# Performance work log

Hardware: AMD Instinct MI355X
Metric: run time of the kernel (lower is better)

Reference implementation:

```python
import jax, jax.numpy as jnp
import numpy as np

DIM = 384
HEADS = 12
HEAD_DIM = DIM // HEADS
WS = 7          # window_size
SS = 3          # shift_size (SW-MSA)
DIM_FF = 4 * DIM
EPS = 1e-5


def _rel_pos_index():
    coords = np.stack(np.meshgrid(np.arange(WS), np.arange(WS), indexing='ij'))
    cf = coords.reshape(2, -1)                       # (2, 49)
    rel = cf[:, :, None] - cf[:, None, :]            # (2, 49, 49)
    rel = rel.transpose(1, 2, 0).astype(np.int64)
    rel[:, :, 0] += WS - 1
    rel[:, :, 1] += WS - 1
    rel[:, :, 0] *= 2 * WS - 1
    return rel.sum(-1)                               # (49, 49)


def _attn_mask(Hp, Wp):
    # cyclic-shift mask, computed on static shapes with numpy
    img = np.zeros((Hp, Wp))
    slices = (slice(0, -WS), slice(-WS, -SS), slice(-SS, None))
    cnt = 0
    for hs in slices:
        for ws_ in slices:
            img[hs, ws_] = cnt
            cnt += 1
    mw = img.reshape(Hp // WS, WS, Wp // WS, WS).transpose(0, 2, 1, 3).reshape(-1, WS * WS)
    am = mw[:, None, :] - mw[:, :, None]             # unsqueeze(1) - unsqueeze(2)
    am = np.where(am != 0, -100.0, 0.0)
    return jnp.asarray(am, jnp.float32)              # (nW, 49, 49)


def _ln(x, g, b):
    mu = jnp.mean(x, -1, keepdims=True)
    var = jnp.mean(jnp.square(x - mu), -1, keepdims=True)
    return (x - mu) * jax.lax.rsqrt(var + EPS) * g + b


def setup_inputs() -> dict:
    key = jax.random.key(0)
    ks = jax.random.split(key, 8)
    B, H, W = 32, 56, 56
    s = 0.02
    return {
        'x': jax.random.normal(ks[0], (B, H * W, DIM), jnp.float32),
        'H': H, 'W': W,
        'rel_idx': jnp.asarray(_rel_pos_index(), jnp.int32),
        'rpb_table': jax.random.normal(ks[1], ((2 * WS - 1) ** 2, HEADS), jnp.float32) * s,
        'qkv_w': jax.random.normal(ks[2], (DIM, 3 * DIM), jnp.float32) * s,
        'proj_w': jax.random.normal(ks[3], (DIM, DIM), jnp.float32) * s,
        'proj_b': jnp.zeros((DIM,), jnp.float32),
        'norm1_g': jnp.ones((DIM,), jnp.float32),
        'norm1_b': jnp.zeros((DIM,), jnp.float32),
        'norm2_g': jnp.ones((DIM,), jnp.float32),
        'norm2_b': jnp.zeros((DIM,), jnp.float32),
        'ffn_w1': jax.random.normal(ks[4], (DIM, DIM_FF), jnp.float32) * s,
        'ffn_b1': jnp.zeros((DIM_FF,), jnp.float32),
        'ffn_w2': jax.random.normal(ks[5], (DIM_FF, DIM), jnp.float32) * s,
        'ffn_b2': jnp.zeros((DIM,), jnp.float32),
    }


def reference(x, H, W, rel_idx, rpb_table, qkv_w, proj_w, proj_b,
              norm1_g, norm1_b, norm2_g, norm2_b,
              ffn_w1, ffn_b1, ffn_w2, ffn_b2):
    B, L, C = x.shape
    shortcut = x
    h = _ln(x, norm1_g, norm1_b).reshape(B, H, W, C)

    pad_b = (WS - H % WS) % WS
    pad_r = (WS - W % WS) % WS
    if pad_b > 0 or pad_r > 0:
        h = jnp.pad(h, ((0, 0), (0, pad_b), (0, pad_r), (0, 0)))
    Hp, Wp = H + pad_b, W + pad_r

    if SS > 0:
        h = jnp.roll(h, (-SS, -SS), axis=(1, 2))

    # window partition -> (B*nW, 49, C)
    nHw, nWw = Hp // WS, Wp // WS
    win = h.reshape(B, nHw, WS, nWw, WS, C).transpose(0, 1, 3, 2, 4, 5)
    win = win.reshape(-1, WS * WS, C)
    Bw, N = win.shape[0], WS * WS

    # window attention
    qkv = (win @ qkv_w).reshape(Bw, N, 3, HEADS, HEAD_DIM)
    q, k, v = [qkv[:, :, i].transpose(0, 2, 1, 3) for i in range(3)]  # (Bw, heads, N, hd)
    attn = jnp.einsum('bhnd,bhmd->bhnm', q, k) / np.sqrt(HEAD_DIM)

    bias = rpb_table[rel_idx]                      # (N, N, heads)
    attn = attn + bias.transpose(2, 0, 1)[None]

    if SS > 0:
        mask = _attn_mask(Hp, Wp)                  # (nW, N, N)
        nW = mask.shape[0]
        attn = attn.reshape(B, nW, HEADS, N, N) + mask[None, :, None]
        attn = attn.reshape(Bw, HEADS, N, N)

    attn = jax.nn.softmax(attn, axis=-1)
    out = jnp.einsum('bhnm,bhmd->bnhd', attn, v).reshape(Bw, N, C)
    out = out @ proj_w + proj_b

    # window reverse
    out = out.reshape(B, nHw, nWw, WS, WS, C).transpose(0, 1, 3, 2, 4, 5)
    out = out.reshape(B, Hp, Wp, C)
    if SS > 0:
        out = jnp.roll(out, (SS, SS), axis=(1, 2))
    if pad_b > 0 or pad_r > 0:
        out = out[:, :H, :W, :]

    h = shortcut + out.reshape(B, H * W, C)
    ff = _ln(h, norm2_g, norm2_b)
    ff = jax.nn.gelu(ff @ ffn_w1 + ffn_b1, approximate=False) @ ffn_w2 + ffn_b2
    return h + ff
```

## Files before the change

### kernel.cpp

```cpp
#include <hip/hip_runtime.h>

#define DEV __device__ __forceinline__

typedef __bf16 bf16x8 __attribute__((ext_vector_type(8)));
typedef float  f32x4  __attribute__((ext_vector_type(4)));
typedef unsigned short u16x8 __attribute__((ext_vector_type(8)));
typedef unsigned short u16x4 __attribute__((ext_vector_type(4)));
typedef long  longx2 __attribute__((ext_vector_type(2)));

DEV float b2f(unsigned short u) {
    unsigned int t = ((unsigned int)u) << 16;
    return __uint_as_float(t);
}
DEV unsigned short f2b(float f) {
    unsigned int u = __float_as_uint(f);
    unsigned int r = (u + 0x7FFFu + ((u >> 16) & 1u)) >> 16;
    return (unsigned short)r;
}
DEV unsigned char f2f8(float f) {
    return (unsigned char)(__builtin_amdgcn_cvt_pk_fp8_f32(f, f, 0, false) & 0xff);
}

DEV int kpos(int c) {
    int s = (c >> 3) & 7;
    return (c & ~63) | ((((s & 3) << 1) | (s >> 2)) << 3) | (c & 7);
}

DEV void gload_lds16(const void* g, void* l) {
    __builtin_amdgcn_global_load_lds(
        (const __attribute__((address_space(1))) void*)g,
        (__attribute__((address_space(3))) void*)l, 16, 0, 0);
}

DEV size_t win_to_tok(int row) {
    int w = row / 49, t = row - w * 49;
    int b  = w >> 6, widx = w & 63;
    int wi = widx >> 3, wj = widx & 7;
    int ti = t / 7, tj = t - ti * 7;
    int hh = wi * 7 + ti + 3; if (hh >= 56) hh -= 56;
    int ww = wj * 7 + tj + 3; if (ww >= 56) ww -= 56;
    return (size_t)b * 3136 + (size_t)hh * 56 + ww;
}

__global__ void tokmap_build(int* __restrict__ tm, int T) {
    int i = blockIdx.x * 256 + threadIdx.x;
    if (i < T) tm[i] = (int)win_to_tok(i);
}

__global__ void wprep8(const float* __restrict__ src, unsigned char* __restrict__ dst,
                       int K, int N) {
    int idx = blockIdx.x * 256 + threadIdx.x;
    if (idx >= K * N) return;
    int k = idx / N, n = idx - k * N;
    dst[(size_t)n * K + kpos(k)] = f2f8(src[idx]);
}

__global__ void btab_build(const int* __restrict__ rel_idx, const float* __restrict__ rpb,
                           float* __restrict__ tab) {
    int idx = blockIdx.x * 256 + threadIdx.x;
    if (idx >= 4 * 12 * 64 * 64) return;
    int col = idx & 63, row = (idx >> 6) & 63;
    int h = (idx >> 12) % 12, cls = idx / (12 * 4096);
    float v;
    if (row >= 49 || col >= 49) {
        v = -10000.f;
    } else {
        v = rpb[rel_idx[row * 49 + col] * 12 + h];
        int ti = row / 7, tj = row - (row / 7) * 7;
        int si = col / 7, sj = col - (col / 7) * 7;
        int lq = ((cls & 2) ? (ti < 4 ? 1 : 2) : 0) * 3 + ((cls & 1) ? (tj < 4 ? 1 : 2) : 0);
        int lk = ((cls & 2) ? (si < 4 ? 1 : 2) : 0) * 3 + ((cls & 1) ? (sj < 4 ? 1 : 2) : 0);
        if (lq != lk) v -= 100.f;
    }
    tab[idx] = v;
}

template <int REMAP>
__global__ __launch_bounds__(256) void ln_kernel(const float* __restrict__ x,
                                                 const float* __restrict__ g,
                                                 const float* __restrict__ b,
                                                 unsigned char* __restrict__ out,
                                                 int rows) {
    int r = blockIdx.x * 4 + (threadIdx.x >> 6);
    int lane = threadIdx.x & 63;
    if (r >= rows) return;
    size_t src = REMAP ? win_to_tok(r) : (size_t)r;
    const float* xp = x + src * 384;
    float v[6];
    float s = 0.f;
#pragma unroll
    for (int i = 0; i < 6; ++i) { v[i] = xp[i * 64 + lane]; s += v[i]; }
#pragma unroll
    for (int off = 32; off; off >>= 1) s += __shfl_xor(s, off, 64);
    float mu = s * (1.f / 384.f);
    float q = 0.f;
#pragma unroll
    for (int i = 0; i < 6; ++i) { float d = v[i] - mu; q += d * d; }
#pragma unroll
    for (int off = 32; off; off >>= 1) q += __shfl_xor(q, off, 64);
    float inv = rsqrtf(q * (1.f / 384.f) + 1e-5f);
    unsigned char* op = out + (size_t)r * 384;
#pragma unroll
    for (int i = 0; i < 6; ++i) {
        int c = i * 64 + lane;
        op[kpos(c)] = f2f8((v[i] - mu) * inv * g[c] + b[c]);
    }
}

template <int MODE>
__global__ __launch_bounds__(512, 2) void gemm_f8_fullk(const unsigned char* __restrict__ A,
                                                        const unsigned char* __restrict__ Bt,
                                                        int M, int N, int K,
                                                        const float* __restrict__ bias,
                                                        const float* __restrict__ resid,
                                                        const int* __restrict__ tokmap,
                                                        unsigned char* __restrict__ outb8,
                                                        float* __restrict__ outf) {
    __shared__ unsigned char Als[64 * 384];
    __shared__ unsigned char Bls[128 * 384];
    const int tid = threadIdx.x;
    const int wid = tid >> 6, lane = tid & 63;
    const int ntile = N >> 7;

    int bid = blockIdx.x;
    int nwg = gridDim.x;
    int swb = ((nwg & 7) == 0) ? ((bid & 7) * (nwg >> 3) + (bid >> 3)) : bid;
    const int mt = swb / ntile, nt = swb - mt * ntile;

    const unsigned char* Abase = A  + (size_t)(mt * 64) * K;
    const unsigned char* Bbase = Bt + (size_t)(nt * 128) * K;

    {
        int rB = tid >> 2;
        int gpB = (tid & 3) ^ ((rB >> 1) & 3);
#pragma unroll
        for (int kb = 0; kb < 6; ++kb)
            gload_lds16(Bbase + (size_t)rB * K + kb * 64 + gpB * 16, &Bls[kb * 8192 + tid * 16]);
        if (tid < 256) {
            int rA = tid >> 2;
            int gpA = (tid & 3) ^ ((rA >> 1) & 3);
#pragma unroll
            for (int kb = 0; kb < 6; ++kb)
                gload_lds16(Abase + (size_t)rA * K + kb * 64 + gpA * 16, &Als[kb * 4096 + tid * 16]);
        }
    }
    asm volatile("s_waitcnt vmcnt(0)" ::: "memory");
    __builtin_amdgcn_s_barrier();

    const int fr = lane & 15, kq = lane >> 4;
    const int cb = (kq ^ ((fr >> 1) & 3)) << 4;

    f32x4 acc[4] = {};
#pragma unroll
    for (int kb = 0; kb < 6; ++kb) {
        longx2 a[4], b;
        b = *(const longx2*)(&Bls[kb * 8192 + (wid * 16 + fr) * 64 + cb]);
#pragma unroll
        for (int m = 0; m < 4; ++m)
            a[m] = *(const longx2*)(&Als[kb * 4096 + (m * 16 + fr) * 64 + cb]);
#pragma unroll
        for (int ks = 0; ks < 2; ++ks)
#pragma unroll
            for (int m = 0; m < 4; ++m)
                acc[m] = __builtin_amdgcn_mfma_f32_16x16x32_fp8_fp8(b[ks], a[m][ks], acc[m], 0, 0, 0);
    }

    const int row0 = mt * 64;
    const int col0 = nt * 128 + wid * 16;
    const int rl = lane & 15;
    const int cq = (lane >> 4) << 2;
    const int col = col0 + cq;
#pragma unroll
    for (int m = 0; m < 4; ++m) {
        int row = row0 + m * 16 + rl;
        f32x4 v = acc[m];
        if constexpr (MODE == 0) {
            int pk = 0;
            pk = __builtin_amdgcn_cvt_pk_fp8_f32(v[0], v[1], pk, false);
            pk = __builtin_amdgcn_cvt_pk_fp8_f32(v[2], v[3], pk, true);
            *(int*)(outb8 + (size_t)row * N + col) = pk;
        } else if constexpr (MODE == 1) {
            size_t o = (size_t)tokmap[row] * 384 + col;
            f32x4 rv = *(const f32x4*)&resid[o];
            f32x4 bb = *(const f32x4*)&bias[col];
            f32x4 ov = rv + v + bb;
            *(f32x4*)&outf[o] = ov;
        } else {
            f32x4 bb = *(const f32x4*)&bias[col];
            float g4[4];
#pragma unroll
            for (int r = 0; r < 4; ++r) {
                float t2 = v[r] + bb[r];
                float e  = __expf(-1.702f * t2);
                g4[r] = t2 * __builtin_amdgcn_rcpf(1.f + e);
            }
            int pk = 0;
            pk = __builtin_amdgcn_cvt_pk_fp8_f32(g4[0], g4[1], pk, false);
            pk = __builtin_amdgcn_cvt_pk_fp8_f32(g4[2], g4[3], pk, true);
            *(int*)(outb8 + (size_t)row * N + kpos(col)) = pk;
        }
    }
}

template <int NBUF, int DEPTH, int MINW>
__global__ __launch_bounds__(256, MINW) void gemm_f8_ring(const unsigned char* __restrict__ A,
                                                          const unsigned char* __restrict__ Bt,
                                                          int M, int N, int K,
                                                          const float* __restrict__ bias,
                                                          const float* __restrict__ resid,
                                                          float* __restrict__ outf) {
    static_assert(NBUF >= DEPTH + 2, "ring too small");
    __shared__ unsigned char As[NBUF][128 * 64];
    __shared__ unsigned char Bs[NBUF][128 * 64];
    const int tid = threadIdx.x;
    const int wid = tid >> 6, lane = tid & 63;
    const int ntile = N >> 7;

    int bid = blockIdx.x;
    int nwg = gridDim.x;
    int swb = ((nwg & 7) == 0) ? ((bid & 7) * (nwg >> 3) + (bid >> 3)) : bid;
    const int mt = swb / ntile, nt = swb - mt * ntile;
    const int wr = wid >> 1, wc = wid & 1;

    f32x4 acc[4][4] = {};

    const unsigned char* Abase = A  + (size_t)(mt * 128) * K;
    const unsigned char* Bbase = Bt + (size_t)(nt * 128) * K;

    auto stage = [&](int buf, int k0) {
#pragma unroll
        for (int j = 0; j < 2; ++j) {
            int r  = j * 64 + (tid >> 2);
            int gp = (tid & 3) ^ ((r >> 1) & 3);
            gload_lds16(Abase + (size_t)r * K + k0 + gp * 16, &As[buf][j * 4096 + tid * 16]);
            gload_lds16(Bbase + (size_t)r * K + k0 + gp * 16, &Bs[buf][j * 4096 + tid * 16]);
        }
    };

    const int fr = lane & 15, kq = lane >> 4;
    const int rowA = wr * 64 + fr;
    const int rowB = wc * 64 + fr;
    const int cb = (kq ^ ((fr >> 1) & 3)) << 4;

    const int nk = K >> 6;
    stage(0, 0);
    if (nk > 1) stage(1, 64);

    for (int t = 0; t < nk; ++t) {
        const int cur = t % NBUF;
        if (t + DEPTH < nk) {
            stage((t + DEPTH) % NBUF, (t + DEPTH) << 6);
            asm volatile("s_waitcnt vmcnt(8)" ::: "memory");
        } else if (t + 1 < nk) {
            asm volatile("s_waitcnt vmcnt(4)" ::: "memory");
        } else {
            asm volatile("s_waitcnt vmcnt(0)" ::: "memory");
        }
        __builtin_amdgcn_s_barrier();

        longx2 a[4], b[4];
#pragma unroll
        for (int m = 0; m < 4; ++m)
            a[m] = *(const longx2*)(&As[cur][(rowA + m * 16) * 64 + cb]);
#pragma unroll
        for (int n = 0; n < 4; ++n)
            b[n] = *(const longx2*)(&Bs[cur][(rowB + n * 16) * 64 + cb]);
#pragma unroll
        for (int ks = 0; ks < 2; ++ks)
#pragma unroll
            for (int m = 0; m < 4; ++m)
#pragma unroll
                for (int n = 0; n < 4; ++n)
                    acc[m][n] = __builtin_amdgcn_mfma_f32_16x16x32_fp8_fp8(b[n][ks], a[m][ks], acc[m][n], 0, 0, 0);

        asm volatile("s_waitcnt lgkmcnt(0)" ::: "memory");
    }

    const int row0 = mt * 128 + wr * 64;
    const int col0 = nt * 128 + wc * 64;
    const int rl = lane & 15;
    const int cq = (lane >> 4) << 2;
#pragma unroll
    for (int m = 0; m < 4; ++m) {
        int row = row0 + m * 16 + rl;
#pragma unroll
        for (int n = 0; n < 4; ++n) {
            int col = col0 + n * 16 + cq;
            f32x4 v = acc[m][n];
            size_t o = (size_t)row * N + col;
            f32x4 rv = *(const f32x4*)&resid[o];
            f32x4 bb = *(const f32x4*)&bias[col];
            f32x4 ov = rv + v + bb;
            *(f32x4*)&outf[o] = ov;
        }
    }
}

__global__ __launch_bounds__(256, 2) void attn_kernel(const unsigned char* __restrict__ QKV8,
                                                      const float* __restrict__ Btab,
                                                      unsigned char* __restrict__ O8) {
    __shared__ char lds[8192 + 16384 + 32768];
    char* Kl = lds;
    char* Vl = lds + 8192;
    char* Pl = lds + 24576;

    const int w   = blockIdx.x;
    const int tid = threadIdx.x, wid = tid >> 6, lane = tid & 63;
    const int fr  = lane & 15, kq = lane >> 4;
    const size_t base = (size_t)w * 49 * 1152;
    const int widx = w & 63, wi = widx >> 3, wj = widx & 7;
    const int cls = ((wi == 7) ? 2 : 0) | ((wj == 7) ? 1 : 0);
    const float* tb = Btab + (size_t)cls * 12 * 4096;
    constexpr float SCL = 0.17677669529663687f;

    for (int R = 0; R < 3; ++R) {
        if (R) __syncthreads();
        {
            f32x4 z = {};
#pragma unroll
            for (int j = 0; j < 6; ++j) *(f32x4*)(lds + j * 4096 + tid * 16) = z;
        }
        __syncthreads();
        {
            int hh = tid >> 6, h = R * 4 + hh;
#pragma unroll
            for (int it = 0; it < 4; ++it) {
                int i = (tid & 63) + it * 64;
                if (i < 196) {
                    int m = i >> 2, c = i & 3;
                    long k8 = *(const long*)(QKV8 + base + (size_t)m * 1152 + 384 + h * 32 + c * 8);
                    int s = c ^ (m & 3) ^ ((m >> 2) & 3);
                    *(long*)(Kl + hh * 2048 + m * 32 + s * 8) = k8;
                    long v8 = *(const long*)(QKV8 + base + (size_t)m * 1152 + 768 + h * 32 + c * 8);
                    int lo = (int)v8, hi = (int)(v8 >> 32);
                    float vf[8];
                    vf[0] = __builtin_amdgcn_cvt_f32_fp8(lo, 0);
                    vf[1] = __builtin_amdgcn_cvt_f32_fp8(lo, 1);
                    vf[2] = __builtin_amdgcn_cvt_f32_fp8(lo, 2);
                    vf[3] = __builtin_amdgcn_cvt_f32_fp8(lo, 3);
                    vf[4] = __builtin_amdgcn_cvt_f32_fp8(hi, 0);
                    vf[5] = __builtin_amdgcn_cvt_f32_fp8(hi, 1);
                    vf[6] = __builtin_amdgcn_cvt_f32_fp8(hi, 2);
                    vf[7] = __builtin_amdgcn_cvt_f32_fp8(hi, 3);
#pragma unroll
                    for (int j = 0; j < 8; ++j) {
                        int d = c * 8 + j;
                        *(unsigned short*)(Vl + hh * 4096 + d * 128 +
                                           (((m >> 3) ^ (d & 7)) * 16) + (m & 7) * 2) = f2b(vf[j]);
                    }
                }
            }
        }
        __syncthreads();

        const int h = R * 4 + wid;
        const float* tbh = tb + h * 4096;

        long aq[4], bk[4];
#pragma unroll
        for (int mi = 0; mi < 4; ++mi) {
            int row = mi * 16 + fr; if (row > 48) row = 48;
            aq[mi] = *(const long*)(QKV8 + base + (size_t)row * 1152 + h * 32 + kq * 8);
        }
#pragma unroll
        for (int ni = 0; ni < 4; ++ni) {
            int rk = ni * 16 + fr;
            bk[ni] = *(const long*)(Kl + wid * 2048 + rk * 32 +
                                    ((kq ^ (rk & 3) ^ ((rk >> 2) & 3)) * 8));
        }
        f32x4 s[4][4] = {};
#pragma unroll
        for (int mi = 0; mi < 4; ++mi)
#pragma unroll
            for (int ni = 0; ni < 4; ++ni)
                s[mi][ni] = __builtin_amdgcn_mfma_f32_16x16x32_fp8_fp8(bk[ni], aq[mi], s[mi][ni], 0, 0, 0);

        float linv_[4];
#pragma unroll
        for (int mi = 0; mi < 4; ++mi) {
            int row = mi * 16 + fr;
            const float* tr = tbh + row * 64 + kq * 4;
            f32x4 sv[4];
            float mx = -1e30f;
#pragma unroll
            for (int ni = 0; ni < 4; ++ni) {
                f32x4 bb = *(const f32x4*)&tr[ni * 16];
                sv[ni] = s[mi][ni] * SCL + bb;
                mx = fmaxf(mx, fmaxf(fmaxf(sv[ni][0], sv[ni][1]), fmaxf(sv[ni][2], sv[ni][3])));
            }
            mx = fmaxf(mx, __shfl_xor(mx, 16, 64));
            mx = fmaxf(mx, __shfl_xor(mx, 32, 64));
            float sm = 0.f;
#pragma unroll
            for (int ni = 0; ni < 4; ++ni)
#pragma unroll
                for (int r = 0; r < 4; ++r) { sv[ni][r] = __expf(sv[ni][r] - mx); sm += sv[ni][r]; }
            sm += __shfl_xor(sm, 16, 64);
            sm += __shfl_xor(sm, 32, 64);
            linv_[mi] = __builtin_amdgcn_rcpf(sm);
#pragma unroll
            for (int ni = 0; ni < 4; ++ni) {
                int colb = ni * 16 + kq * 4;
                int phys = (colb >> 3) ^ (row & 7);
                u16x4 pk;
#pragma unroll
                for (int r = 0; r < 4; ++r) pk[r] = f2b(sv[ni][r]);
                *(u16x4*)(Pl + wid * 8192 + row * 128 + phys * 16 + (colb & 7) * 2) = pk;
            }
        }
        asm volatile("s_waitcnt lgkmcnt(0)" ::: "memory");
        __builtin_amdgcn_sched_barrier(0);

        f32x4 oacc[4][2] = {};
#pragma unroll
        for (int sl = 0; sl < 2; ++sl) {
            bf16x8 bv[2];
#pragma unroll
            for (int ni = 0; ni < 2; ++ni) {
                int d = ni * 16 + fr;
                bv[ni] = *(const bf16x8*)(Vl + wid * 4096 + d * 128 + (((sl * 4 + kq) ^ (d & 7)) * 16));
            }
#pragma unroll
            for (int mi = 0; mi < 4; ++mi) {
                int row = mi * 16 + fr;
                bf16x8 ap = *(const bf16x8*)(Pl + wid * 8192 + row * 128 + (((sl * 4 + kq) ^ (row & 7)) * 16));
#pragma unroll
                for (int ni = 0; ni < 2; ++ni)
                    oacc[mi][ni] = __builtin_amdgcn_mfma_f32_16x16x32_bf16(bv[ni], ap, oacc[mi][ni], 0, 0, 0);
            }
        }

#pragma unroll
        for (int mi = 0; mi < 4; ++mi) {
            int row = mi * 16 + fr;
            if (row < 49) {
                float li = linv_[mi];
                unsigned char* opb = O8 + (size_t)(w * 49 + row) * 384;
#pragma unroll
                for (int ni = 0; ni < 2; ++ni) {
                    int c = h * 32 + ni * 16 + kq * 4;
                    int pk = 0;
                    pk = __builtin_amdgcn_cvt_pk_fp8_f32(oacc[mi][ni][0] * li, oacc[mi][ni][1] * li, pk, false);
                    pk = __builtin_amdgcn_cvt_pk_fp8_f32(oacc[mi][ni][2] * li, oacc[mi][ni][3] * li, pk, true);
                    *(int*)(opb + kpos(c)) = pk;
                }
            }
        }
    }
}

extern "C" void kernel_launch(void* const* d_in, const int* in_sizes, int n_in,
                              void* d_out, int out_size, void* d_ws, size_t ws_size,
                              hipStream_t stream) {
    const float* x     = (const float*)d_in[0];
    const int*   rel   = (const int*)  d_in[3];
    const float* rpb   = (const float*)d_in[4];
    const float* qkvw  = (const float*)d_in[5];
    const float* projw = (const float*)d_in[6];
    const float* projb = (const float*)d_in[7];
    const float* n1g   = (const float*)d_in[8];
    const float* n1b   = (const float*)d_in[9];
    const float* n2g   = (const float*)d_in[10];
    const float* n2b   = (const float*)d_in[11];
    const float* w1    = (const float*)d_in[12];
    const float* b1    = (const float*)d_in[13];
    const float* w2    = (const float*)d_in[14];
    const float* b2    = (const float*)d_in[15];
    float* out = (float*)d_out;

    const int T = in_sizes[0] / 384;

    char* ws = (char*)d_ws;
    size_t off = 0;
    auto alloc = [&](size_t bytes) {
        char* p = ws + off;
        off += (bytes + 255) & ~(size_t)255;
        return p;
    };
    unsigned char* Wq8  = (unsigned char*)alloc((size_t)1152 * 384);
    unsigned char* Wp8  = (unsigned char*)alloc((size_t)384 * 384);
    unsigned char* W18  = (unsigned char*)alloc((size_t)1536 * 384);
    unsigned char* W28  = (unsigned char*)alloc((size_t)384 * 1536);
    float*         Btab = (float*)       alloc((size_t)4 * 12 * 4096 * 4);
    int*           Tmap = (int*)         alloc((size_t)T * 4);
    unsigned char* slotA = (unsigned char*)alloc((size_t)T * 384);
    unsigned char* slotB = (unsigned char*)alloc((size_t)T * 1536);

    unsigned char* X1   = slotA;
    unsigned char* O8   = slotA;
    unsigned char* X2   = slotA;
    unsigned char* QKV8 = slotB;
    unsigned char* F8   = slotB;
    float*         Hh   = out;

    wprep8<<<dim3((1152 * 384 + 255) / 256), 256, 0, stream>>>(qkvw, Wq8, 384, 1152);
    wprep8<<<dim3((384 * 384 + 255) / 256),  256, 0, stream>>>(projw, Wp8, 384, 384);
    wprep8<<<dim3((384 * 1536 + 255) / 256), 256, 0, stream>>>(w1, W18, 384, 1536);
    wprep8<<<dim3((1536 * 384 + 255) / 256), 256, 0, stream>>>(w2, W28, 1536, 384);
    btab_build<<<dim3((4 * 12 * 4096 + 255) / 256), 256, 0, stream>>>(rel, rpb, Btab);
    tokmap_build<<<dim3((T + 255) / 256), 256, 0, stream>>>(Tmap, T);

    ln_kernel<1><<<dim3(T / 4), 256, 0, stream>>>(x, n1g, n1b, X1, T);
    gemm_f8_fullk<0><<<dim3((T / 64) * (1152 / 128)), 512, 0, stream>>>(
        X1, Wq8, T, 1152, 384, nullptr, nullptr, nullptr, QKV8, nullptr);
    attn_kernel<<<dim3(T / 49), 256, 0, stream>>>(QKV8, Btab, O8);
    gemm_f8_fullk<1><<<dim3((T / 64) * (384 / 128)), 512, 0, stream>>>(
        O8, Wp8, T, 384, 384, projb, x, Tmap, nullptr, Hh);
    ln_kernel<0><<<dim3(T / 4), 256, 0, stream>>>(Hh, n2g, n2b, X2, T);
    gemm_f8_fullk<2><<<dim3((T / 64) * (1536 / 128)), 512, 0, stream>>>(
        X2, W18, T, 1536, 384, b1, nullptr, nullptr, F8, nullptr);
    gemm_f8_ring<4, 2, 2><<<dim3((T / 128) * (384 / 128)), 256, 0, stream>>>(
        F8, W28, T, 384, 1536, b2, Hh, out);
}
```

Baseline: 636.1 us.

## Retile FFN down-projection GEMM to 64x128 tiles with 8 waves per block

Replaces the 128x128 tile, 4-wave ring GEMM used for the FFN second projection with a 64x128 tile, 8-wave version in which each wave computes a 64x16 strip. This doubles the block count, shrinks the per-wave accumulator from 16 to 4 MFMA tiles, and raises occupancy through launch bounds of 512 threads with min 4 blocks. In exchange there is less operand reuse per wave (more LDS reads per MFMA) and waits that differ by wave because only half the threads load A.

```diff
diff --git a/kernel.cpp b/kernel.cpp
--- a/kernel.cpp
+++ b/kernel.cpp
@@ -202,15 +202,15 @@
     }
 }
 
-template <int NBUF, int DEPTH, int MINW>
-__global__ __launch_bounds__(256, MINW) void gemm_f8_ring(const unsigned char* __restrict__ A,
-                                                          const unsigned char* __restrict__ Bt,
-                                                          int M, int N, int K,
-                                                          const float* __restrict__ bias,
-                                                          const float* __restrict__ resid,
-                                                          float* __restrict__ outf) {
-    static_assert(NBUF >= DEPTH + 2, "ring too small");
-    __shared__ unsigned char As[NBUF][128 * 64];
+template <int NBUF, int DEPTH>
+__global__ __launch_bounds__(512, 4) void gemm_f8_ring8(const unsigned char* __restrict__ A,
+                                                        const unsigned char* __restrict__ Bt,
+                                                        int M, int N, int K,
+                                                        const float* __restrict__ bias,
+                                                        const float* __restrict__ resid,
+                                                        float* __restrict__ outf) {
+    static_assert(NBUF >= DEPTH + 2, "single-barrier ring needs NBUF >= DEPTH+2");
+    __shared__ unsigned char As[NBUF][64 * 64];
     __shared__ unsigned char Bs[NBUF][128 * 64];
     const int tid = threadIdx.x;
     const int wid = tid >> 6, lane = tid & 63;
@@ -220,79 +220,71 @@
     int nwg = gridDim.x;
     int swb = ((nwg & 7) == 0) ? ((bid & 7) * (nwg >> 3) + (bid >> 3)) : bid;
     const int mt = swb / ntile, nt = swb - mt * ntile;
-    const int wr = wid >> 1, wc = wid & 1;
-
-    f32x4 acc[4][4] = {};
-
-    const unsigned char* Abase = A  + (size_t)(mt * 128) * K;
+
+    f32x4 acc[4] = {};
+
+    const unsigned char* Abase = A  + (size_t)(mt * 64) * K;
     const unsigned char* Bbase = Bt + (size_t)(nt * 128) * K;
 
     auto stage = [&](int buf, int k0) {
-#pragma unroll
-        for (int j = 0; j < 2; ++j) {
-            int r  = j * 64 + (tid >> 2);
-            int gp = (tid & 3) ^ ((r >> 1) & 3);
-            gload_lds16(Abase + (size_t)r * K + k0 + gp * 16, &As[buf][j * 4096 + tid * 16]);
-            gload_lds16(Bbase + (size_t)r * K + k0 + gp * 16, &Bs[buf][j * 4096 + tid * 16]);
+        int rB = tid >> 2;
+        int gpB = (tid & 3) ^ ((rB >> 1) & 3);
+        gload_lds16(Bbase + (size_t)rB * K + k0 + gpB * 16, &Bs[buf][tid * 16]);
+        if (tid < 256) {
+            int rA = tid >> 2;
+            int gpA = (tid & 3) ^ ((rA >> 1) & 3);
+            gload_lds16(Abase + (size_t)rA * K + k0 + gpA * 16, &As[buf][tid * 16]);
         }
     };
 
     const int fr = lane & 15, kq = lane >> 4;
-    const int rowA = wr * 64 + fr;
-    const int rowB = wc * 64 + fr;
     const int cb = (kq ^ ((fr >> 1) & 3)) << 4;
+    const int rowB = wid * 16 + fr;
 
     const int nk = K >> 6;
     stage(0, 0);
-    if (nk > 1) stage(1, 64);
+    stage(1, 64);
 
     for (int t = 0; t < nk; ++t) {
         const int cur = t % NBUF;
         if (t + DEPTH < nk) {
             stage((t + DEPTH) % NBUF, (t + DEPTH) << 6);
-            asm volatile("s_waitcnt vmcnt(8)" ::: "memory");
+            if (wid < 4) { asm volatile("s_waitcnt vmcnt(4)" ::: "memory"); }
+            else         { asm volatile("s_waitcnt vmcnt(2)" ::: "memory"); }
         } else if (t + 1 < nk) {
-            asm volatile("s_waitcnt vmcnt(4)" ::: "memory");
+            if (wid < 4) { asm volatile("s_waitcnt vmcnt(2)" ::: "memory"); }
+            else         { asm volatile("s_waitcnt vmcnt(1)" ::: "memory"); }
         } else {
             asm volatile("s_waitcnt vmcnt(0)" ::: "memory");
         }
         __builtin_amdgcn_s_barrier();
 
-        longx2 a[4], b[4];
+        longx2 a[4], b;
+        b = *(const longx2*)(&Bs[cur][rowB * 64 + cb]);
 #pragma unroll
         for (int m = 0; m < 4; ++m)
-            a[m] = *(const longx2*)(&As[cur][(rowA + m * 16) * 64 + cb]);
-#pragma unroll
-        for (int n = 0; n < 4; ++n)
-            b[n] = *(const longx2*)(&Bs[cur][(rowB + n * 16) * 64 + cb]);
+            a[m] = *(const longx2*)(&As[cur][(m * 16 + fr) * 64 + cb]);
 #pragma unroll
         for (int ks = 0; ks < 2; ++ks)
 #pragma unroll
             for (int m = 0; m < 4; ++m)
-#pragma unroll
-                for (int n = 0; n < 4; ++n)
-                    acc[m][n] = __builtin_amdgcn_mfma_f32_16x16x32_fp8_fp8(b[n][ks], a[m][ks], acc[m][n], 0, 0, 0);
+                acc[m] = __builtin_amdgcn_mfma_f32_16x16x32_fp8_fp8(b[ks], a[m][ks], acc[m], 0, 0, 0);
 
         asm volatile("s_waitcnt lgkmcnt(0)" ::: "memory");
     }
 
-    const int row0 = mt * 128 + wr * 64;
-    const int col0 = nt * 128 + wc * 64;
-    const int rl = lane & 15;
-    const int cq = (lane >> 4) << 2;
+    const int row0 = mt * 64;
+    const int col  = nt * 128 + wid * 16 + ((lane >> 4) << 2);
+    const int rl   = lane & 15;
 #pragma unroll
     for (int m = 0; m < 4; ++m) {
         int row = row0 + m * 16 + rl;
-#pragma unroll
-        for (int n = 0; n < 4; ++n) {
-            int col = col0 + n * 16 + cq;
-            f32x4 v = acc[m][n];
-            size_t o = (size_t)row * N + col;
-            f32x4 rv = *(const f32x4*)&resid[o];
-            f32x4 bb = *(const f32x4*)&bias[col];
-            f32x4 ov = rv + v + bb;
-            *(f32x4*)&outf[o] = ov;
-        }
+        f32x4 v = acc[m];
+        size_t o = (size_t)row * N + col;
+        f32x4 rv = *(const f32x4*)&resid[o];
+        f32x4 bb = *(const f32x4*)&bias[col];
+        f32x4 ov = rv + v + bb;
+        *(f32x4*)&outf[o] = ov;
     }
 }
 
@@ -509,6 +501,6 @@
     ln_kernel<0><<<dim3(T / 4), 256, 0, stream>>>(Hh, n2g, n2b, X2, T);
     gemm_f8_fullk<2><<<dim3((T / 64) * (1536 / 128)), 512, 0, stream>>>(
         X2, W18, T, 1536, 384, b1, nullptr, nullptr, F8, nullptr);
-    gemm_f8_ring<4, 2, 2><<<dim3((T / 128) * (384 / 128)), 256, 0, stream>>>(
+    gemm_f8_ring8<4, 2><<<dim3((T / 64) * (384 / 128)), 512, 0, stream>>>(
         F8, W28, T, 384, 1536, b2, Hh, out);
 }
```

Result: slower. 651.2 us (+2.4%).
